# Kernel tuning notes

Measured on AMD Instinct MI355X. Metric: run time of the kernel, lower is better.

The kernel has to match this reference:

```python
import jax, jax.numpy as jnp
import numpy as np

B, L, D, H, HD, FF, NL = 2, 2048, 1024, 16, 64, 4096, 2
EPS = 1e-5
NEG = -1e30


def setup_inputs() -> dict:
    key = jax.random.key(0)
    ks = jax.random.split(key, 20)
    x = jax.random.normal(ks[0], (B, L, D), jnp.float32)
    # RoPE tables, rotate-half convention: [L, HD]
    pos = jnp.arange(L, dtype=jnp.float32)
    freqs = 1.0 / (10000.0 ** (jnp.arange(0, HD, 2, dtype=jnp.float32) / HD))
    ang = pos[:, None] * freqs[None, :]              # [L, HD/2]
    cos = jnp.concatenate([jnp.cos(ang), jnp.cos(ang)], -1)
    sin = jnp.concatenate([jnp.sin(ang), jnp.sin(ang)], -1)
    s = 0.02
    wq = jax.random.normal(ks[1], (NL, D, D), jnp.float32) * s
    wk = jax.random.normal(ks[2], (NL, D, D), jnp.float32) * s
    wv = jax.random.normal(ks[3], (NL, D, D), jnp.float32) * s
    wo = jax.random.normal(ks[4], (NL, D, D), jnp.float32) * s
    w1 = jax.random.normal(ks[5], (NL, D, FF), jnp.float32) * s
    w2 = jax.random.normal(ks[6], (NL, FF, D), jnp.float32) * s
    w3 = jax.random.normal(ks[7], (NL, D, FF), jnp.float32) * s
    attn_norm = jnp.ones((NL, D), jnp.float32)
    mlp_norm = jnp.ones((NL, D), jnp.float32)
    final_norm = jnp.ones((D,), jnp.float32)
    rw1 = jax.random.normal(ks[8], (D, D), jnp.float32) * s
    rb1 = jnp.zeros((D,), jnp.float32)
    rw2 = jax.random.normal(ks[9], (D, 1), jnp.float32) * s
    rb2 = jnp.zeros((1,), jnp.float32)
    return dict(x=x, cos=cos, sin=sin, wq=wq, wk=wk, wv=wv, wo=wo,
                w1=w1, w2=w2, w3=w3, attn_norm=attn_norm, mlp_norm=mlp_norm,
                final_norm=final_norm, rw1=rw1, rb1=rb1, rw2=rw2, rb2=rb2)


def _rms(x, w):
    return x * jax.lax.rsqrt(jnp.mean(x * x, -1, keepdims=True) + EPS) * w


def _rope(t, cos, sin):
    # t: [B, L, H, HD]; cos/sin: [L, HD]
    t1, t2 = jnp.split(t, 2, axis=-1)
    rot = jnp.concatenate([-t2, t1], -1)
    return t * cos[None, :, None, :] + rot * sin[None, :, None, :]


def reference(x, cos, sin, wq, wk, wv, wo, w1, w2, w3,
              attn_norm, mlp_norm, final_norm, rw1, rb1, rw2, rb2):
    causal = jnp.tril(jnp.ones((L, L), bool))
    h = x
    for i in range(NL):  # small fixed layer loop
        a = _rms(h, attn_norm[i])
        q = _rope((a @ wq[i]).reshape(B, L, H, HD), cos, sin)
        k = _rope((a @ wk[i]).reshape(B, L, H, HD), cos, sin)
        v = (a @ wv[i]).reshape(B, L, H, HD)
        sc = jnp.einsum('bqhd,bkhd->bhqk', q, k) / np.float32(np.sqrt(HD))
        sc = jnp.where(causal, sc, NEG)
        o = jnp.einsum('bhqk,bkhd->bqhd', jax.nn.softmax(sc, -1), v)
        h = h + o.reshape(B, L, D) @ wo[i]
        m = _rms(h, mlp_norm[i])
        h = h + (jax.nn.silu(m @ w1[i]) * (m @ w3[i])) @ w2[i]
    h = _rms(h, final_norm)

    # router chunking: straight-through hard boundaries
    logits = (jax.nn.silu(h @ rw1 + rb1) @ rw2 + rb2)[..., 0]   # [B, L]
    probs = jax.nn.sigmoid(logits)
    hard = (probs > 0.5).astype(h.dtype)
    mask = probs + jax.lax.stop_gradient(hard - probs)
    mask = mask.at[:, 0].set(1.0)
    mhard = jax.lax.stop_gradient(mask)
    # select matrix: S padded to static upper bound L (rows >= counts are zero)
    cums = jnp.cumsum(mhard, -1)                                # [B, L]
    seg = jnp.arange(1, L + 1, dtype=cums.dtype)[None, :, None] # [1, S, 1]
    assignment = (cums[:, None, :] == seg).astype(h.dtype)      # [B, S, L]
    select = assignment * mask[:, None, :]
    compressed = jnp.einsum('bsl,bld->bsd', select, h)          # [B, S, D]
    boundary_positions = jnp.argsort(-mhard, axis=-1)           # stable in jax
    counts = mhard.sum(-1).astype(jnp.int32)
    avg_chunk_size = jnp.float32(L) / jnp.mean(counts.astype(jnp.float32))
    return (h, compressed, boundary_positions, counts, avg_chunk_size)
```

## Files before the change

### kernel.cpp

```cpp
#include <hip/hip_runtime.h>
#include <cmath>

#define B_  2
#define L_  2048
#define D_  1024
#define H_  16
#define FF_ 4096
#define NL_ 2
#define NT_ (B_*L_)
#define ND_ (NT_*D_)

typedef __attribute__((ext_vector_type(8))) short bf16x8;
typedef __attribute__((ext_vector_type(4))) float f32x4;

__device__ __forceinline__ short f2bf(float x){
  unsigned u = __builtin_bit_cast(unsigned, x);
  unsigned r = (u + 0x7fffu + ((u>>16)&1u)) >> 16;
  return (short)r;
}
__device__ __forceinline__ float bf2f(short s){
  unsigned u = ((unsigned)(unsigned short)s) << 16;
  return __builtin_bit_cast(float, u);
}
#define MFMA16(a,b,c) __builtin_amdgcn_mfma_f32_16x16x32_bf16(a,b,c,0,0,0)

__device__ __forceinline__ void gload16(const short* g, short* l){
  __builtin_amdgcn_global_load_lds((const __attribute__((address_space(1))) void*)g,
                                   (__attribute__((address_space(3))) void*)l, 16, 0, 0);
}

__device__ __forceinline__ int2 xcd_swizzle(){
  int gx = gridDim.x;
  int n  = gx * gridDim.y;
  int hw = blockIdx.x + gx*blockIdx.y;
  int logical = (hw&7)*(n>>3) + (hw>>3);
  return make_int2(logical % gx, logical / gx);
}

template<bool WF32>
__global__ __launch_bounds__(256) void k_rmsnorm_s(const float* __restrict__ in,
                                                   const float* __restrict__ w,
                                                   short* __restrict__ oh,
                                                   short* __restrict__ ol,
                                                   float* __restrict__ of){
  int row = blockIdx.x; int tid = threadIdx.x;
  float4 xv = ((const float4*)(in + (size_t)row*D_))[tid];
  float ss = xv.x*xv.x + xv.y*xv.y + xv.z*xv.z + xv.w*xv.w;
  #pragma unroll
  for (int off=32; off; off>>=1) ss += __shfl_xor(ss, off);
  __shared__ float wsum[4];
  if ((tid&63)==0) wsum[tid>>6] = ss;
  __syncthreads();
  float tot = wsum[0]+wsum[1]+wsum[2]+wsum[3];
  float scale = 1.0f / sqrtf(tot*(1.0f/(float)D_) + 1e-5f);
  float4 w4 = ((const float4*)w)[tid];
  float v[4] = {xv.x*scale*w4.x, xv.y*scale*w4.y, xv.z*scale*w4.z, xv.w*scale*w4.w};
  short4 hh, ll;
  short h0=f2bf(v[0]); hh.x=h0; ll.x=f2bf(v[0]-bf2f(h0));
  short h1=f2bf(v[1]); hh.y=h1; ll.y=f2bf(v[1]-bf2f(h1));
  short h2=f2bf(v[2]); hh.z=h2; ll.z=f2bf(v[2]-bf2f(h2));
  short h3=f2bf(v[3]); hh.w=h3; ll.w=f2bf(v[3]-bf2f(h3));
  *(short4*)(oh + (size_t)row*D_ + tid*4) = hh;
  *(short4*)(ol + (size_t)row*D_ + tid*4) = ll;
  if (WF32){
    float4 ov; ov.x=v[0]; ov.y=v[1]; ov.z=v[2]; ov.w=v[3];
    ((float4*)(of + (size_t)row*D_))[tid] = ov;
  }
}

__global__ __launch_bounds__(256) void k_wsplit(const float* __restrict__ src,
                                                short* __restrict__ dh,
                                                short* __restrict__ dl,
                                                int srcN, int kOff, int nOff, int KT){
  __shared__ float t[64][68];
  int k0 = blockIdx.x*64, n0v = blockIdx.y*64;
  int tid = threadIdx.x;
  #pragma unroll
  for (int p=0;p<4;p++){
    int r = p*16 + (tid>>4);
    int c4 = (tid&15)*4;
    float4 v = *(const float4*)(src + (size_t)(kOff + k0 + r)*srcN + nOff + n0v + c4);
    *(float4*)&t[r][c4] = v;
  }
  __syncthreads();
  int n = tid>>2, kk = (tid&3)*16;
  bf16x8 H0, L0, H1, L1;
  #pragma unroll
  for (int q=0;q<8;q++){
    float v = t[kk+q][n]; short h=f2bf(v); H0[q]=h; L0[q]=f2bf(v-bf2f(h));
  }
  #pragma unroll
  for (int q=0;q<8;q++){
    float v = t[kk+8+q][n]; short h=f2bf(v); H1[q]=h; L1[q]=f2bf(v-bf2f(h));
  }
  size_t dof = (size_t)(n0v + n)*KT + k0 + kk;
  *(bf16x8*)(dh + dof) = H0;  *(bf16x8*)(dh + dof + 8) = H1;
  *(bf16x8*)(dl + dof) = L0;  *(bf16x8*)(dl + dof + 8) = L1;
}

__global__ __launch_bounds__(256,2) void k_qkv_mm(const short* __restrict__ Ah,
                                                  const short* __restrict__ Al,
                                                  const short* __restrict__ Wh,
                                                  const short* __restrict__ Wl,
                                                  short* __restrict__ OutH){
  __shared__ short lds[32768];
  int tid = threadIdx.x, wid = tid>>6, lane = tid&63;
  int l15 = lane&15, l4 = lane>>4;
  int wr = wid>>1, wc = wid&1;
  int2 bxy = xcd_swizzle();
  int m0 = bxy.y*128, n0 = bxy.x*128;
  const int K = 1024;
  f32x4 acc[4][4];
  #pragma unroll
  for (int i=0;i<4;i++){
    #pragma unroll
    for (int j=0;j<4;j++) acc[i][j] = (f32x4){0.f,0.f,0.f,0.f};
  }
  const short* gsrc = (wid==0)?Ah:(wid==1)?Al:(wid==2)?Wh:Wl;
  int rb = (wid<2)? m0 : n0;
  int gcol = ((lane&7)^(lane>>3))*8;
  short* ldsw = lds + wid*8192;
  const short* gp0 = gsrc + (size_t)(rb + (lane>>3))*K + gcol;
  for (int k0=0; k0<K; k0+=64){
    const short* gp = gp0 + k0;
    #pragma unroll
    for (int lc=0; lc<16; ++lc)
      gload16(gp + (size_t)lc*8*K, ldsw + lc*512);
    __syncthreads();
    #pragma unroll
    for (int ks=0; ks<2; ++ks){
      bf16x8 af[4], alf[4], wf[4], wlf[4];
      int gs = ((ks*4 + l4) ^ (lane&7))*8;
      #pragma unroll
      for (int f=0; f<4; ++f){
        int ar = (wr*64 + f*16 + l15)*64 + gs;
        af[f]  = *(const bf16x8*)&lds[ar];
        alf[f] = *(const bf16x8*)&lds[8192 + ar];
        int wr2 = (wc*64 + f*16 + l15)*64 + gs;
        wf[f]  = *(const bf16x8*)&lds[16384 + wr2];
        wlf[f] = *(const bf16x8*)&lds[24576 + wr2];
      }
      __builtin_amdgcn_s_setprio(1);
      #pragma unroll
      for (int i=0;i<4;i++){
        #pragma unroll
        for (int j=0;j<4;j++){
          acc[i][j] = MFMA16(af[i],  wf[j],  acc[i][j]);
          acc[i][j] = MFMA16(alf[i], wf[j],  acc[i][j]);
          acc[i][j] = MFMA16(af[i],  wlf[j], acc[i][j]);
        }
      }
      __builtin_amdgcn_s_setprio(0);
    }
    __syncthreads();
  }
  int sel = n0 >> 10;
  short* oh = OutH + (size_t)sel*8388608;
  short* ol = oh + 4194304;
  int cb = (n0 & 1023) + wc*64;
  #pragma unroll
  for (int i=0;i<4;i++){
    #pragma unroll
    for (int j=0;j<4;j++){
      #pragma unroll
      for (int r=0;r<4;r++){
        size_t mg = (size_t)(m0 + wr*64 + i*16 + l4*4 + r);
        int ng = cb + j*16 + l15;
        float v = acc[i][j][r];
        short h = f2bf(v);
        oh[mg*1024 + ng] = h;
        ol[mg*1024 + ng] = f2bf(v - bf2f(h));
      }
    }
  }
}

template<int EPI>
__global__ __launch_bounds__(256,(EPI==3)?2:3) void k_mm64(const short* __restrict__ Ah,
                                                const short* __restrict__ Al,
                                                const short* __restrict__ Wh,
                                                const short* __restrict__ Wl,
                                                const short* __restrict__ W3h,
                                                const short* __restrict__ W3l,
                                                int K,
                                                float* __restrict__ Cf,
                                                const float* __restrict__ bias,
                                                short* __restrict__ Gh,
                                                short* __restrict__ Gl,
                                                int ldc){
  __shared__ short lds[(EPI==3)?32768:24576];
  int tid = threadIdx.x, wid = tid>>6, lane = tid&63;
  int l15 = lane&15, l4 = lane>>4;
  int2 bxy = xcd_swizzle();
  int m0 = bxy.y*128, n0 = bxy.x*64;
  f32x4 a1[2][4], a3[2][4];
  #pragma unroll
  for (int i=0;i<2;i++){
    #pragma unroll
    for (int j=0;j<4;j++){ a1[i][j]=(f32x4){0.f,0.f,0.f,0.f}; a3[i][j]=(f32x4){0.f,0.f,0.f,0.f}; }
  }
  int gcol = ((lane&7)^(lane>>3))*8;
  int l8 = lane>>3;
  const int NCH = (EPI==3)? 16 : 12;
  for (int k0=0; k0<K; k0+=64){
    for (int t=0; t<NCH; ++t){
      int c = wid*NCH + t;
      const short* sb; int row0; short* db;
      if (c < 32){
        sb = (c<16)? Ah : Al; row0 = m0 + (c&15)*8;
        db = lds + ((c<16)?0:8192) + (c&15)*512;
      } else {
        int wseg = (c-32)>>3;
        sb = (wseg==0)?Wh:(wseg==1)?Wl:(wseg==2)?W3h:W3l;
        row0 = n0 + (c&7)*8;
        db = lds + 16384 + wseg*4096 + (c&7)*512;
      }
      gload16(sb + (size_t)(row0 + l8)*K + k0 + gcol, db);
    }
    __syncthreads();
    #pragma unroll
    for (int ks=0; ks<2; ++ks){
      int gs = ((ks*4 + l4) ^ (lane&7))*8;
      bf16x8 af[2], alf[2], wh[4], wl[4];
      #pragma unroll
      for (int f=0; f<2; ++f){
        int ar = (wid*32 + f*16 + l15)*64 + gs;
        af[f]  = *(const bf16x8*)&lds[ar];
        alf[f] = *(const bf16x8*)&lds[8192 + ar];
      }
      #pragma unroll
      for (int f=0; f<4; ++f){
        int wr2 = (f*16 + l15)*64 + gs;
        wh[f] = *(const bf16x8*)&lds[16384 + wr2];
        wl[f] = *(const bf16x8*)&lds[20480 + wr2];
      }
      __builtin_amdgcn_s_setprio(1);
      #pragma unroll
      for (int i=0;i<2;i++){
        #pragma unroll
        for (int j=0;j<4;j++){
          a1[i][j] = MFMA16(af[i],  wh[j], a1[i][j]);
          a1[i][j] = MFMA16(alf[i], wh[j], a1[i][j]);
          a1[i][j] = MFMA16(af[i],  wl[j], a1[i][j]);
        }
      }
      __builtin_amdgcn_s_setprio(0);
      if (EPI==3){
        bf16x8 w3h[4], w3l[4];
        #pragma unroll
        for (int f=0; f<4; ++f){
          int wr2 = (f*16 + l15)*64 + gs;
          w3h[f] = *(const bf16x8*)&lds[24576 + wr2];
          w3l[f] = *(const bf16x8*)&lds[28672 + wr2];
        }
        __builtin_amdgcn_s_setprio(1);
        #pragma unroll
        for (int i=0;i<2;i++){
          #pragma unroll
          for (int j=0;j<4;j++){
            a3[i][j] = MFMA16(af[i],  w3h[j], a3[i][j]);
            a3[i][j] = MFMA16(alf[i], w3h[j], a3[i][j]);
            a3[i][j] = MFMA16(af[i],  w3l[j], a3[i][j]);
          }
        }
        __builtin_amdgcn_s_setprio(0);
      }
    }
    __syncthreads();
  }
  #pragma unroll
  for (int i=0;i<2;i++){
    #pragma unroll
    for (int j=0;j<4;j++){
      #pragma unroll
      for (int r=0;r<4;r++){
        size_t mg = (size_t)(m0 + wid*32 + i*16 + l4*4 + r);
        int ng = n0 + j*16 + l15;
        float v = a1[i][j][r];
        if (EPI==1){
          float* cp = Cf + mg*ldc + ng;
          *cp = *cp + v;
        } else if (EPI==2){
          float x = v + bias[ng];
          Cf[mg*ldc + ng] = x/(1.f+expf(-x));
        } else {
          float g = v/(1.f+expf(-v)) * a3[i][j][r];
          short h = f2bf(g);
          Gh[mg*2048 + ng] = h;
          Gl[mg*2048 + ng] = f2bf(g - bf2f(h));
        }
      }
    }
  }
}

__global__ __launch_bounds__(256) void k_prep_k(const short* __restrict__ kh,
                                                const short* __restrict__ kl,
                                                const float* __restrict__ cosT,
                                                const float* __restrict__ sinT,
                                                short* __restrict__ kf){
  int wave = threadIdx.x>>6, lane = threadIdx.x&63;
  int t16 = blockIdx.x*4 + wave;
  int bh = blockIdx.y; int b = bh>>4, h = bh&15;
  int l15 = lane&15, l4 = lane>>4;
  int tok = t16*16 + l15;
  const short* khp = kh + (size_t)(b*L_+tok)*D_ + h*64;
  const short* klp = kl + (size_t)(b*L_+tok)*D_ + h*64;
  int d0 = l4*8;
  bf16x8 ka  = *(const bf16x8*)(khp + d0);
  bf16x8 kb2 = *(const bf16x8*)(khp + 32 + d0);
  bf16x8 kla = *(const bf16x8*)(klp + d0);
  bf16x8 klb = *(const bf16x8*)(klp + 32 + d0);
  const float* cr = cosT + (size_t)tok*64;
  const float* sr = sinT + (size_t)tok*64;
  float c0[8], s0[8], c1[8], s1[8];
  *(float4*)&c0[0] = *(const float4*)(cr + d0);      *(float4*)&c0[4] = *(const float4*)(cr + d0 + 4);
  *(float4*)&c1[0] = *(const float4*)(cr + 32 + d0); *(float4*)&c1[4] = *(const float4*)(cr + 32 + d0 + 4);
  *(float4*)&s0[0] = *(const float4*)(sr + d0);      *(float4*)&s0[4] = *(const float4*)(sr + d0 + 4);
  *(float4*)&s1[0] = *(const float4*)(sr + 32 + d0); *(float4*)&s1[4] = *(const float4*)(sr + 32 + d0 + 4);
  bf16x8 h0, lo0, h1, lo1;
  #pragma unroll
  for (int j=0;j<8;j++){
    float k0v = bf2f(ka[j]) + bf2f(kla[j]);
    float k1v = bf2f(kb2[j]) + bf2f(klb[j]);
    float r0 = k0v*c0[j] - k1v*s0[j];
    float r1 = k1v*c1[j] + k0v*s1[j];
    short a = f2bf(r0); h0[j]=a; lo0[j]=f2bf(r0 - bf2f(a));
    short bS = f2bf(r1); h1[j]=bS; lo1[j]=f2bf(r1 - bf2f(bS));
  }
  size_t base = ((size_t)(bh*128 + t16)*4)*512 + lane*8;
  *(bf16x8*)(kf + base)        = h0;
  *(bf16x8*)(kf + base + 512)  = lo0;
  *(bf16x8*)(kf + base + 1024) = h1;
  *(bf16x8*)(kf + base + 1536) = lo1;
}

__global__ __launch_bounds__(256) void k_prep_v(const short* __restrict__ vh,
                                                const short* __restrict__ vl,
                                                short* __restrict__ vf){
  int wave = threadIdx.x>>6, lane = threadIdx.x&63;
  int kc = blockIdx.x;
  int bh = blockIdx.y; int b = bh>>4, h = bh&15;
  int dt = wave;
  int l15 = lane&15, l4 = lane>>4;
  bf16x8 hi, lo;
  #pragma unroll
  for (int i=0;i<8;i++){
    size_t off = (size_t)(b*L_ + kc*32 + l4*8 + i)*D_ + h*64 + dt*16 + l15;
    hi[i] = vh[off];
    lo[i] = vl[off];
  }
  size_t base = (((size_t)(bh*64 + kc)*4 + dt)*2)*512 + lane*8;
  *(bf16x8*)(vf + base)       = hi;
  *(bf16x8*)(vf + base + 512) = lo;
}

__global__ __launch_bounds__(256) void k_attn_mfma(const short* __restrict__ qhb,
                                                   const short* __restrict__ qlb,
                                                   const short* __restrict__ kf,
                                                   const short* __restrict__ vf,
                                                   const float* __restrict__ cosT,
                                                   const float* __restrict__ sinT,
                                                   short* __restrict__ oh,
                                                   short* __restrict__ ol){
  int bid = blockIdx.x;
  int logical = (bid&7)*64 + (bid>>3);
  int bh = logical>>4, pair = logical&15;
  int b = bh>>4, h = bh&15;
  int wave = threadIdx.x>>6, lane = threadIdx.x&63;
  int l15 = lane&15, l4 = lane>>4;
  __shared__ short kvs[2][16384];
  __shared__ short pblob[4][2048];
  short* pb = pblob[wave];

  auto stage = [&](int bufi, int kt){
    const short* kg = kf + ((size_t)(bh*128 + kt*4))*2048;
    const short* vg = vf + ((size_t)(bh*64 + kt*2))*4096;
    short* dst = kvs[bufi];
    #pragma unroll
    for (int c=0;c<8;c++){
      int ch = wave*8 + c;
      const short* src = (ch<16)? (kg + ch*512) : (vg + (ch-16)*512);
      gload16(src + lane*8, dst + ch*512);
    }
  };

  for (int half=0; half<2; ++half){
    int qt = (half==0) ? (31-pair) : pair;
    stage(0, 0);
    int tok = qt*64 + wave*16 + l15;
    const short* qhp = qhb + (size_t)(b*L_+tok)*D_ + h*64;
    const short* qlp = qlb + (size_t)(b*L_+tok)*D_ + h*64;
    int d0 = l4*8;
    bf16x8 qa  = *(const bf16x8*)(qhp + d0);
    bf16x8 qb2 = *(const bf16x8*)(qhp + 32 + d0);
    bf16x8 qla = *(const bf16x8*)(qlp + d0);
    bf16x8 qlb2= *(const bf16x8*)(qlp + 32 + d0);
    const float* cr = cosT + (size_t)tok*64;
    const float* sr = sinT + (size_t)tok*64;
    float c0[8], s0[8], c1[8], s1[8];
    *(float4*)&c0[0] = *(const float4*)(cr + d0);      *(float4*)&c0[4] = *(const float4*)(cr + d0 + 4);
    *(float4*)&c1[0] = *(const float4*)(cr + 32 + d0); *(float4*)&c1[4] = *(const float4*)(cr + 32 + d0 + 4);
    *(float4*)&s0[0] = *(const float4*)(sr + d0);      *(float4*)&s0[4] = *(const float4*)(sr + d0 + 4);
    *(float4*)&s1[0] = *(const float4*)(sr + 32 + d0); *(float4*)&s1[4] = *(const float4*)(sr + 32 + d0 + 4);
    bf16x8 qh0, ql0, qh1, ql1;
    #pragma unroll
    for (int j=0;j<8;j++){
      float q0v = bf2f(qa[j]) + bf2f(qla[j]);
      float q1v = bf2f(qb2[j]) + bf2f(qlb2[j]);
      float r0 = (q0v*c0[j] - q1v*s0[j]) * 0.125f;
      float r1 = (q1v*c1[j] + q0v*s1[j]) * 0.125f;
      short a = f2bf(r0); qh0[j]=a; ql0[j]=f2bf(r0 - bf2f(a));
      short bS = f2bf(r1); qh1[j]=bS; ql1[j]=f2bf(r1 - bf2f(bS));
    }

    f32x4 O[4];
    #pragma unroll
    for (int dt=0;dt<4;dt++) O[dt] = (f32x4){0.f,0.f,0.f,0.f};
    float m_[4] = {-1e30f,-1e30f,-1e30f,-1e30f};
    float ls[4] = {0.f,0.f,0.f,0.f};

    int cur = 0;
    for (int kt=0; kt<=qt; ++kt){
      bool haveNext = (kt < qt);
      if (haveNext){
        stage(cur^1, kt+1);
        asm volatile("s_waitcnt vmcnt(8)" ::: "memory");
      } else {
        asm volatile("s_waitcnt vmcnt(0)" ::: "memory");
      }
      __builtin_amdgcn_s_barrier();
      const short* Kl = kvs[cur];
      const short* Vl = kvs[cur] + 8192;
      bool dtile = (kt == qt);
      f32x4 sr4[4];
      #pragma unroll
      for (int g=0; g<4; g++){
        f32x4 acc = (f32x4){0.f,0.f,0.f,0.f};
        if (!(dtile && g > wave)){
          const short* kp = Kl + g*2048 + lane*8;
          bf16x8 kh0 = *(const bf16x8*)(kp);
          bf16x8 kl0 = *(const bf16x8*)(kp + 512);
          bf16x8 kh1 = *(const bf16x8*)(kp + 1024);
          bf16x8 kl1 = *(const bf16x8*)(kp + 1536);
          __builtin_amdgcn_s_setprio(1);
          acc = MFMA16(qh0, kh0, acc); acc = MFMA16(qh1, kh1, acc);
          acc = MFMA16(ql0, kh0, acc); acc = MFMA16(ql1, kh1, acc);
          acc = MFMA16(qh0, kl0, acc); acc = MFMA16(qh1, kl1, acc);
          __builtin_amdgcn_s_setprio(0);
        }
        sr4[g] = acc;
      }
      float p_[4][4];
      #pragma unroll
      for (int r=0; r<4; r++){
        int rowrel = wave*16 + l4*4 + r;
        float mx = -1e30f;
        float sv[4];
        #pragma unroll
        for (int g=0; g<4; g++){
          float v = sr4[g][r];
          if (dtile && (g*16 + l15) > rowrel) v = -1e30f;
          sv[g] = v; mx = fmaxf(mx, v);
        }
        #pragma unroll
        for (int off=1; off<16; off<<=1) mx = fmaxf(mx, __shfl_xor(mx, off));
        float nm = fmaxf(m_[r], mx);
        float al = __expf(m_[r] - nm);
        m_[r] = nm;
        float ps = 0.f;
        #pragma unroll
        for (int g=0; g<4; g++){ float pv = __expf(sv[g] - nm); p_[g][r] = pv; ps += pv; }
        #pragma unroll
        for (int off=1; off<16; off<<=1) ps += __shfl_xor(ps, off);
        ls[r] = ls[r]*al + ps;
        #pragma unroll
        for (int dt=0; dt<4; dt++) O[dt][r] *= al;
      }
      #pragma unroll
      for (int g=0; g<4; g++){
        int key = g*16 + l15;
        int cc = key>>5, sub = (key>>3)&3, ii = key&7;
        #pragma unroll
        for (int r=0; r<4; r++){
          float pv = p_[g][r];
          short ph = f2bf(pv);
          short pl = f2bf(pv - bf2f(ph));
          int idx = cc*1024 + (sub*16 + l4*4 + r)*8 + ii;
          pb[idx] = ph;
          pb[idx + 512] = pl;
        }
      }
      asm volatile("s_waitcnt lgkmcnt(0)" ::: "memory");
      #pragma unroll
      for (int cc=0; cc<2; cc++){
        bf16x8 pah = *(const bf16x8*)(pb + cc*1024 + lane*8);
        bf16x8 pal = *(const bf16x8*)(pb + cc*1024 + 512 + lane*8);
        const short* vp = Vl + cc*4096 + lane*8;
        __builtin_amdgcn_s_setprio(1);
        #pragma unroll
        for (int dt=0; dt<4; dt++){
          bf16x8 vh = *(const bf16x8*)(vp + dt*1024);
          bf16x8 vl = *(const bf16x8*)(vp + dt*1024 + 512);
          O[dt] = MFMA16(pah, vh, O[dt]);
          O[dt] = MFMA16(pal, vh, O[dt]);
          O[dt] = MFMA16(pah, vl, O[dt]);
        }
        __builtin_amdgcn_s_setprio(0);
      }
      __builtin_amdgcn_s_barrier();
      cur ^= 1;
    }
    #pragma unroll
    for (int r=0; r<4; r++){
      float inv = 1.0f / ls[r];
      size_t row = (size_t)(b*L_ + qt*64 + wave*16 + l4*4 + r);
      #pragma unroll
      for (int dt=0; dt<4; dt++){
        float v = O[dt][r]*inv;
        short hh = f2bf(v);
        oh[row*D_ + h*64 + dt*16 + l15] = hh;
        ol[row*D_ + h*64 + dt*16 + l15] = f2bf(v - bf2f(hh));
      }
    }
  }
}

__global__ __launch_bounds__(256) void k_gemv(const float* __restrict__ T,
                                              const float* __restrict__ rw2,
                                              const float* __restrict__ rb2,
                                              float* __restrict__ logits){
  int row = blockIdx.x; int tid = threadIdx.x;
  float4 tv = ((const float4*)(T + (size_t)row*D_))[tid];
  float4 wv = ((const float4*)rw2)[tid];
  float s = tv.x*wv.x + tv.y*wv.y + tv.z*wv.z + tv.w*wv.w;
  #pragma unroll
  for (int off=32; off; off>>=1) s += __shfl_xor(s, off);
  __shared__ float ps[4];
  if ((tid&63)==0) ps[tid>>6] = s;
  __syncthreads();
  if (tid==0) logits[row] = ps[0]+ps[1]+ps[2]+ps[3] + rb2[0];
}

__global__ __launch_bounds__(256) void k_boundary(const float* __restrict__ logits,
                                                  float* __restrict__ pos_out,
                                                  int* __restrict__ hard,
                                                  int* __restrict__ cums,
                                                  int* __restrict__ counts){
  int b = blockIdx.x; int tid = threadIdx.x;
  __shared__ int part[256];
  int loc[8]; int s=0;
  int base = b*L_;
  #pragma unroll
  for (int j=0;j<8;j++){
    int ll = tid*8 + j;
    float lg = logits[base+ll];
    int hv = (ll==0) ? 1 : ((lg > 0.0f) ? 1 : 0);
    loc[j]=hv; s+=hv;
  }
  part[tid]=s; __syncthreads();
  for (int off=1; off<256; off<<=1){
    int v = part[tid];
    int add = (tid>=off) ? part[tid-off] : 0;
    __syncthreads();
    part[tid] = v + add;
    __syncthreads();
  }
  int total = part[255];
  int run = part[tid] - s;
  #pragma unroll
  for (int j=0;j<8;j++){
    int ll = tid*8+j;
    run += loc[j];
    hard[base+ll] = loc[j];
    cums[base+ll] = run;
    int idx = loc[j] ? (run-1) : (total + ll - run);
    pos_out[base+idx] = (float)ll;
  }
  if (tid==0) counts[b] = total;
}

__global__ __launch_bounds__(256) void k_scatter(const float* __restrict__ hf,
                                                 const int* __restrict__ hard,
                                                 const int* __restrict__ cums,
                                                 float* __restrict__ comp){
  int rowid = blockIdx.x;
  if (!hard[rowid]) return;
  int b = rowid >> 11;
  int s = cums[rowid]-1;
  const float4* src = (const float4*)(hf + (size_t)rowid*D_);
  float4* dst = (float4*)(comp + (size_t)(b*L_ + s)*D_);
  dst[threadIdx.x] = src[threadIdx.x];
}

__global__ void k_finalize(const int* __restrict__ counts, float* __restrict__ out){
  if (threadIdx.x==0 && blockIdx.x==0){
    float c0 = (float)counts[0], c1 = (float)counts[1];
    out[0]=c0; out[1]=c1;
    out[2] = (float)L_ / (0.5f*(c0+c1));
  }
}

extern "C" void kernel_launch(void* const* d_in, const int* in_sizes, int n_in,
                              void* d_out, int out_size, void* d_ws, size_t ws_size,
                              hipStream_t stream){
  const float* x      = (const float*)d_in[0];
  const float* cosT   = (const float*)d_in[1];
  const float* sinT   = (const float*)d_in[2];
  const float* wq     = (const float*)d_in[3];
  const float* wk     = (const float*)d_in[4];
  const float* wv     = (const float*)d_in[5];
  const float* wo     = (const float*)d_in[6];
  const float* w1     = (const float*)d_in[7];
  const float* w2     = (const float*)d_in[8];
  const float* w3     = (const float*)d_in[9];
  const float* attn_n = (const float*)d_in[10];
  const float* mlp_n  = (const float*)d_in[11];
  const float* final_n= (const float*)d_in[12];
  const float* rw1    = (const float*)d_in[13];
  const float* rb1    = (const float*)d_in[14];
  const float* rw2    = (const float*)d_in[15];
  const float* rb2    = (const float*)d_in[16];

  float* outF = (float*)d_out;
  float* hD   = outF;
  float* compD= outF + (size_t)ND_;
  float* posD = outF + (size_t)2*ND_;

  char* WS = (char*)d_ws;
  auto S = [&](size_t mb){ return (short*)(WS + mb*1048576ull); };
  auto F = [&](size_t mb){ return (float*)(WS + mb*1048576ull); };
  short *ah=S(0), *al=S(8);
  short *qh=S(16), *ql=S(24), *kh=S(32), *kl=S(40), *vh=S(48), *vl=S(56);
  short *qkvwt_h=S(64), *qkvwt_l=S(70);
  short *vf=S(64);
  short *kf=S(48);
  short *wot_h=S(32), *wot_l=S(34);
  short *gh=S(16), *gl=S(32);
  short *w1t_h=S(48), *w1t_l=S(52), *w3t_h=S(56), *w3t_l=S(60);
  short *w2t_h=S(64), *w2t_l=S(68);
  short *rw1t_h=S(16), *rw1t_l=S(18);
  float *ra=F(20);
  float *logits=F(76);
  int *hard=(int*)(logits+NT_), *cums=hard+NT_, *cnts=cums+NT_;
  short *oh=(short*)compD, *ol=oh+4194304;

  hipMemcpyAsync(hD, x, (size_t)ND_*sizeof(float), hipMemcpyDeviceToDevice, stream);

  for (int i=0;i<NL_;++i){
    k_rmsnorm_s<false><<<NT_,256,0,stream>>>(hD, attn_n + (size_t)i*D_, ah, al, nullptr);
    k_wsplit<<<dim3(16,16),256,0,stream>>>(wq + (size_t)i*D_*D_, qkvwt_h,         qkvwt_l,         1024, 0, 0, 1024);
    k_wsplit<<<dim3(16,16),256,0,stream>>>(wk + (size_t)i*D_*D_, qkvwt_h+1048576, qkvwt_l+1048576, 1024, 0, 0, 1024);
    k_wsplit<<<dim3(16,16),256,0,stream>>>(wv + (size_t)i*D_*D_, qkvwt_h+2097152, qkvwt_l+2097152, 1024, 0, 0, 1024);
    k_qkv_mm<<<dim3(24,32),256,0,stream>>>(ah, al, qkvwt_h, qkvwt_l, qh);
    k_prep_v<<<dim3(64,32),256,0,stream>>>(vh, vl, vf);
    k_prep_k<<<dim3(32,32),256,0,stream>>>(kh, kl, cosT, sinT, kf);
    k_wsplit<<<dim3(16,16),256,0,stream>>>(wo + (size_t)i*D_*D_, wot_h, wot_l, 1024, 0, 0, 1024);
    k_attn_mfma<<<dim3(512),256,0,stream>>>(qh, ql, kf, vf, cosT, sinT, oh, ol);
    k_mm64<1><<<dim3(16,32),256,0,stream>>>(oh, ol, wot_h, wot_l, nullptr, nullptr,
                                            1024, hD, nullptr, nullptr, nullptr, 1024);
    k_rmsnorm_s<false><<<NT_,256,0,stream>>>(hD, mlp_n + (size_t)i*D_, ah, al, nullptr);
    for (int hc=0; hc<2; ++hc){
      k_wsplit<<<dim3(16,32),256,0,stream>>>(w1 + (size_t)i*D_*FF_, w1t_h, w1t_l, 4096, 0, hc*2048, 1024);
      k_wsplit<<<dim3(16,32),256,0,stream>>>(w3 + (size_t)i*D_*FF_, w3t_h, w3t_l, 4096, 0, hc*2048, 1024);
      k_wsplit<<<dim3(32,16),256,0,stream>>>(w2 + (size_t)i*FF_*D_, w2t_h, w2t_l, 1024, hc*2048, 0, 2048);
      k_mm64<3><<<dim3(32,32),256,0,stream>>>(ah, al, w1t_h, w1t_l, w3t_h, w3t_l,
                                              1024, nullptr, nullptr, gh, gl, 0);
      k_mm64<1><<<dim3(16,32),256,0,stream>>>(gh, gl, w2t_h, w2t_l, nullptr, nullptr,
                                              2048, hD, nullptr, nullptr, nullptr, 1024);
    }
  }
  k_rmsnorm_s<true><<<NT_,256,0,stream>>>(hD, final_n, ah, al, hD);
  k_wsplit<<<dim3(16,16),256,0,stream>>>(rw1, rw1t_h, rw1t_l, 1024, 0, 0, 1024);
  k_mm64<2><<<dim3(16,32),256,0,stream>>>(ah, al, rw1t_h, rw1t_l, nullptr, nullptr,
                                          1024, ra, rb1, nullptr, nullptr, 1024);
  k_gemv<<<NT_,256,0,stream>>>(ra, rw2, rb2, logits);
  k_boundary<<<B_,256,0,stream>>>(logits, posD, hard, cums, cnts);
  hipMemsetAsync(compD, 0, (size_t)ND_*sizeof(float), stream);
  k_scatter<<<NT_,256,0,stream>>>(hD, hard, cums, compD);
  k_finalize<<<1,64,0,stream>>>(cnts, posD + NT_);
}
```

Measured before the change: 1.256 ms.

## Batch weight-split launches, fuse V layout into QKV GEMM, lazy softmax rescale

Merges the separate weight-split launches (QKV, FFN, and Wo together with K preparation) into single grid launches, which cuts launch overhead and lets small kernels overlap. The V output of the QKV GEMM is now written directly in the attention layout, so the k_prep_v kernel and its round trip through memory are gone. Attention softmax skips the running-max rescale when the new block max stays within 8 of the current max, which saves exp and multiply work. Launch-bound occupancy hints are also raised, which risks register spills, and workspace buffers are remapped to avoid aliasing.

```diff
diff --git a/kernel.cpp b/kernel.cpp
--- a/kernel.cpp
+++ b/kernel.cpp
@@ -68,41 +68,80 @@
   }
 }
 
+__device__ __forceinline__ void wsplit_body(float (*t)[68], const float* __restrict__ src,
+                                            short* __restrict__ dh, short* __restrict__ dl,
+                                            int srcN, int kOff, int nOff, int KT,
+                                            int bx, int by){
+  int k0 = bx*64, n0v = by*64;
+  int tid = threadIdx.x;
+  #pragma unroll
+  for (int p=0;p<4;p++){
+    int r = p*16 + (tid>>4);
+    int c4 = (tid&15)*4;
+    float4 v = *(const float4*)(src + (size_t)(kOff + k0 + r)*srcN + nOff + n0v + c4);
+    *(float4*)&t[r][c4] = v;
+  }
+  __syncthreads();
+  int n = tid>>2, kk = (tid&3)*16;
+  bf16x8 H0, L0, H1, L1;
+  #pragma unroll
+  for (int q=0;q<8;q++){
+    float v = t[kk+q][n]; short h=f2bf(v); H0[q]=h; L0[q]=f2bf(v-bf2f(h));
+  }
+  #pragma unroll
+  for (int q=0;q<8;q++){
+    float v = t[kk+8+q][n]; short h=f2bf(v); H1[q]=h; L1[q]=f2bf(v-bf2f(h));
+  }
+  size_t dof = (size_t)(n0v + n)*KT + k0 + kk;
+  *(bf16x8*)(dh + dof) = H0;  *(bf16x8*)(dh + dof + 8) = H1;
+  *(bf16x8*)(dl + dof) = L0;  *(bf16x8*)(dl + dof + 8) = L1;
+}
+
 __global__ __launch_bounds__(256) void k_wsplit(const float* __restrict__ src,
                                                 short* __restrict__ dh,
                                                 short* __restrict__ dl,
                                                 int srcN, int kOff, int nOff, int KT){
   __shared__ float t[64][68];
-  int k0 = blockIdx.x*64, n0v = blockIdx.y*64;
-  int tid = threadIdx.x;
-  #pragma unroll
-  for (int p=0;p<4;p++){
-    int r = p*16 + (tid>>4);
-    int c4 = (tid&15)*4;
-    float4 v = *(const float4*)(src + (size_t)(kOff + k0 + r)*srcN + nOff + n0v + c4);
-    *(float4*)&t[r][c4] = v;
-  }
-  __syncthreads();
-  int n = tid>>2, kk = (tid&3)*16;
-  bf16x8 H0, L0, H1, L1;
-  #pragma unroll
-  for (int q=0;q<8;q++){
-    float v = t[kk+q][n]; short h=f2bf(v); H0[q]=h; L0[q]=f2bf(v-bf2f(h));
-  }
-  #pragma unroll
-  for (int q=0;q<8;q++){
-    float v = t[kk+8+q][n]; short h=f2bf(v); H1[q]=h; L1[q]=f2bf(v-bf2f(h));
-  }
-  size_t dof = (size_t)(n0v + n)*KT + k0 + kk;
-  *(bf16x8*)(dh + dof) = H0;  *(bf16x8*)(dh + dof + 8) = H1;
-  *(bf16x8*)(dl + dof) = L0;  *(bf16x8*)(dl + dof + 8) = L1;
-}
-
-__global__ __launch_bounds__(256,2) void k_qkv_mm(const short* __restrict__ Ah,
+  wsplit_body(t, src, dh, dl, srcN, kOff, nOff, KT, blockIdx.x, blockIdx.y);
+}
+
+__global__ __launch_bounds__(256) void k_wsplit_qkv(const float* __restrict__ wq,
+                                                    const float* __restrict__ wk,
+                                                    const float* __restrict__ wv,
+                                                    short* __restrict__ dh,
+                                                    short* __restrict__ dl){
+  __shared__ float t[64][68];
+  int z = blockIdx.z;
+  const float* s = (z==0)?wq:(z==1)?wk:wv;
+  wsplit_body(t, s, dh + (size_t)z*1048576, dl + (size_t)z*1048576,
+              1024, 0, 0, 1024, blockIdx.x, blockIdx.y);
+}
+
+__global__ __launch_bounds__(256) void k_wsplit_ffn(const float* __restrict__ w1,
+                                                    const float* __restrict__ w3,
+                                                    const float* __restrict__ w2,
+                                                    short* __restrict__ w1h, short* __restrict__ w1l,
+                                                    short* __restrict__ w3h, short* __restrict__ w3l,
+                                                    short* __restrict__ w2h, short* __restrict__ w2l,
+                                                    int hc){
+  __shared__ float t[64][68];
+  int z = blockIdx.z;
+  if (z < 2){
+    if (blockIdx.x >= 16) return;
+    const float* s = z ? w3 : w1;
+    wsplit_body(t, s, z?w3h:w1h, z?w3l:w1l, 4096, 0, hc*2048, 1024, blockIdx.x, blockIdx.y);
+  } else {
+    if (blockIdx.y >= 16) return;
+    wsplit_body(t, w2, w2h, w2l, 1024, hc*2048, 0, 2048, blockIdx.x, blockIdx.y);
+  }
+}
+
+__global__ __launch_bounds__(256,3) void k_qkv_mm(const short* __restrict__ Ah,
                                                   const short* __restrict__ Al,
                                                   const short* __restrict__ Wh,
                                                   const short* __restrict__ Wl,
-                                                  short* __restrict__ OutH){
+                                                  short* __restrict__ OutH,
+                                                  short* __restrict__ Vf){
   __shared__ short lds[32768];
   int tid = threadIdx.x, wid = tid>>6, lane = tid&63;
   int l15 = lane&15, l4 = lane>>4;
@@ -155,28 +194,52 @@
     __syncthreads();
   }
   int sel = n0 >> 10;
-  short* oh = OutH + (size_t)sel*8388608;
-  short* ol = oh + 4194304;
   int cb = (n0 & 1023) + wc*64;
-  #pragma unroll
-  for (int i=0;i<4;i++){
-    #pragma unroll
-    for (int j=0;j<4;j++){
-      #pragma unroll
-      for (int r=0;r<4;r++){
-        size_t mg = (size_t)(m0 + wr*64 + i*16 + l4*4 + r);
-        int ng = cb + j*16 + l15;
-        float v = acc[i][j][r];
-        short h = f2bf(v);
-        oh[mg*1024 + ng] = h;
-        ol[mg*1024 + ng] = f2bf(v - bf2f(h));
+  if (sel < 2){
+    short* oh = OutH + (size_t)sel*8388608;
+    short* ol = oh + 4194304;
+    #pragma unroll
+    for (int i=0;i<4;i++){
+      #pragma unroll
+      for (int j=0;j<4;j++){
+        #pragma unroll
+        for (int r=0;r<4;r++){
+          size_t mg = (size_t)(m0 + wr*64 + i*16 + l4*4 + r);
+          int ng = cb + j*16 + l15;
+          float v = acc[i][j][r];
+          short h = f2bf(v);
+          oh[mg*1024 + ng] = h;
+          ol[mg*1024 + ng] = f2bf(v - bf2f(h));
+        }
+      }
+    }
+  } else {
+    #pragma unroll
+    for (int i=0;i<4;i++){
+      #pragma unroll
+      for (int j=0;j<4;j++){
+        #pragma unroll
+        for (int r=0;r<4;r++){
+          int mg = m0 + wr*64 + i*16 + l4*4 + r;
+          int ng = cb + j*16 + l15;
+          float v = acc[i][j][r];
+          short hh2 = f2bf(v);
+          short ll2 = f2bf(v - bf2f(hh2));
+          int bb = mg >> 11, tt = mg & 2047;
+          int hd = ng >> 6, kc = tt >> 5;
+          int l4v = (tt>>3)&3, iv = tt&7;
+          int dtv = (ng>>4)&3, l15v = ng&15;
+          size_t base = ((size_t)((bb*16+hd)*64 + kc)*8 + dtv*2)*512 + (l4v*16+l15v)*8 + iv;
+          Vf[base] = hh2;
+          Vf[base + 512] = ll2;
+        }
       }
     }
   }
 }
 
 template<int EPI>
-__global__ __launch_bounds__(256,(EPI==3)?2:3) void k_mm64(const short* __restrict__ Ah,
+__global__ __launch_bounds__(256,(EPI==3)?3:4) void k_mm64(const short* __restrict__ Ah,
                                                 const short* __restrict__ Al,
                                                 const short* __restrict__ Wh,
                                                 const short* __restrict__ Wl,
@@ -294,14 +357,24 @@
   }
 }
 
-__global__ __launch_bounds__(256) void k_prep_k(const short* __restrict__ kh,
-                                                const short* __restrict__ kl,
-                                                const float* __restrict__ cosT,
-                                                const float* __restrict__ sinT,
-                                                short* __restrict__ kf){
+__global__ __launch_bounds__(256) void k_prep_k_wo(const short* __restrict__ kh,
+                                                   const short* __restrict__ kl,
+                                                   const float* __restrict__ cosT,
+                                                   const float* __restrict__ sinT,
+                                                   short* __restrict__ kf,
+                                                   const float* __restrict__ wo,
+                                                   short* __restrict__ woh,
+                                                   short* __restrict__ wol){
+  __shared__ float t[64][68];
+  int x = blockIdx.x;
+  if (x >= 1024){
+    int idx = x - 1024;
+    wsplit_body(t, wo, woh, wol, 1024, 0, 0, 1024, idx & 15, idx >> 4);
+    return;
+  }
   int wave = threadIdx.x>>6, lane = threadIdx.x&63;
-  int t16 = blockIdx.x*4 + wave;
-  int bh = blockIdx.y; int b = bh>>4, h = bh&15;
+  int t16 = (x & 31)*4 + wave;
+  int bh = x >> 5; int b = bh>>4, h = bh&15;
   int l15 = lane&15, l4 = lane>>4;
   int tok = t16*16 + l15;
   const short* khp = kh + (size_t)(b*L_+tok)*D_ + h*64;
@@ -333,26 +406,6 @@
   *(bf16x8*)(kf + base + 512)  = lo0;
   *(bf16x8*)(kf + base + 1024) = h1;
   *(bf16x8*)(kf + base + 1536) = lo1;
-}
-
-__global__ __launch_bounds__(256) void k_prep_v(const short* __restrict__ vh,
-                                                const short* __restrict__ vl,
-                                                short* __restrict__ vf){
-  int wave = threadIdx.x>>6, lane = threadIdx.x&63;
-  int kc = blockIdx.x;
-  int bh = blockIdx.y; int b = bh>>4, h = bh&15;
-  int dt = wave;
-  int l15 = lane&15, l4 = lane>>4;
-  bf16x8 hi, lo;
-  #pragma unroll
-  for (int i=0;i<8;i++){
-    size_t off = (size_t)(b*L_ + kc*32 + l4*8 + i)*D_ + h*64 + dt*16 + l15;
-    hi[i] = vh[off];
-    lo[i] = vl[off];
-  }
-  size_t base = (((size_t)(bh*64 + kc)*4 + dt)*2)*512 + lane*8;
-  *(bf16x8*)(vf + base)       = hi;
-  *(bf16x8*)(vf + base + 512) = lo;
 }
 
 __global__ __launch_bounds__(256) void k_attn_mfma(const short* __restrict__ qhb,
@@ -465,17 +518,26 @@
         }
         #pragma unroll
         for (int off=1; off<16; off<<=1) mx = fmaxf(mx, __shfl_xor(mx, off));
-        float nm = fmaxf(m_[r], mx);
-        float al = __expf(m_[r] - nm);
-        m_[r] = nm;
-        float ps = 0.f;
-        #pragma unroll
-        for (int g=0; g<4; g++){ float pv = __expf(sv[g] - nm); p_[g][r] = pv; ps += pv; }
-        #pragma unroll
-        for (int off=1; off<16; off<<=1) ps += __shfl_xor(ps, off);
-        ls[r] = ls[r]*al + ps;
-        #pragma unroll
-        for (int dt=0; dt<4; dt++) O[dt][r] *= al;
+        if (__all(mx <= m_[r] + 8.0f)){
+          float ps = 0.f;
+          #pragma unroll
+          for (int g=0; g<4; g++){ float pv = __expf(sv[g] - m_[r]); p_[g][r] = pv; ps += pv; }
+          #pragma unroll
+          for (int off=1; off<16; off<<=1) ps += __shfl_xor(ps, off);
+          ls[r] += ps;
+        } else {
+          float nm = fmaxf(m_[r], mx);
+          float al = __expf(m_[r] - nm);
+          m_[r] = nm;
+          float ps = 0.f;
+          #pragma unroll
+          for (int g=0; g<4; g++){ float pv = __expf(sv[g] - nm); p_[g][r] = pv; ps += pv; }
+          #pragma unroll
+          for (int off=1; off<16; off<<=1) ps += __shfl_xor(ps, off);
+          ls[r] = ls[r]*al + ps;
+          #pragma unroll
+          for (int dt=0; dt<4; dt++) O[dt][r] *= al;
+        }
       }
       #pragma unroll
       for (int g=0; g<4; g++){
@@ -631,11 +693,11 @@
   auto S = [&](size_t mb){ return (short*)(WS + mb*1048576ull); };
   auto F = [&](size_t mb){ return (float*)(WS + mb*1048576ull); };
   short *ah=S(0), *al=S(8);
-  short *qh=S(16), *ql=S(24), *kh=S(32), *kl=S(40), *vh=S(48), *vl=S(56);
-  short *qkvwt_h=S(64), *qkvwt_l=S(70);
+  short *qh=S(16), *ql=S(24), *kh=S(32), *kl=S(40);
+  short *qkvwt_h=S(48), *qkvwt_l=S(54);
   short *vf=S(64);
   short *kf=S(48);
-  short *wot_h=S(32), *wot_l=S(34);
+  short *wot_h=S(0), *wot_l=S(2);
   short *gh=S(16), *gl=S(32);
   short *w1t_h=S(48), *w1t_l=S(52), *w3t_h=S(56), *w3t_l=S(60);
   short *w2t_h=S(64), *w2t_l=S(68);
@@ -649,21 +711,19 @@
 
   for (int i=0;i<NL_;++i){
     k_rmsnorm_s<false><<<NT_,256,0,stream>>>(hD, attn_n + (size_t)i*D_, ah, al, nullptr);
-    k_wsplit<<<dim3(16,16),256,0,stream>>>(wq + (size_t)i*D_*D_, qkvwt_h,         qkvwt_l,         1024, 0, 0, 1024);
-    k_wsplit<<<dim3(16,16),256,0,stream>>>(wk + (size_t)i*D_*D_, qkvwt_h+1048576, qkvwt_l+1048576, 1024, 0, 0, 1024);
-    k_wsplit<<<dim3(16,16),256,0,stream>>>(wv + (size_t)i*D_*D_, qkvwt_h+2097152, qkvwt_l+2097152, 1024, 0, 0, 1024);
-    k_qkv_mm<<<dim3(24,32),256,0,stream>>>(ah, al, qkvwt_h, qkvwt_l, qh);
-    k_prep_v<<<dim3(64,32),256,0,stream>>>(vh, vl, vf);
-    k_prep_k<<<dim3(32,32),256,0,stream>>>(kh, kl, cosT, sinT, kf);
-    k_wsplit<<<dim3(16,16),256,0,stream>>>(wo + (size_t)i*D_*D_, wot_h, wot_l, 1024, 0, 0, 1024);
+    k_wsplit_qkv<<<dim3(16,16,3),256,0,stream>>>(wq + (size_t)i*D_*D_, wk + (size_t)i*D_*D_,
+                                                 wv + (size_t)i*D_*D_, qkvwt_h, qkvwt_l);
+    k_qkv_mm<<<dim3(24,32),256,0,stream>>>(ah, al, qkvwt_h, qkvwt_l, qh, vf);
+    k_prep_k_wo<<<dim3(1280),256,0,stream>>>(kh, kl, cosT, sinT, kf,
+                                             wo + (size_t)i*D_*D_, wot_h, wot_l);
     k_attn_mfma<<<dim3(512),256,0,stream>>>(qh, ql, kf, vf, cosT, sinT, oh, ol);
     k_mm64<1><<<dim3(16,32),256,0,stream>>>(oh, ol, wot_h, wot_l, nullptr, nullptr,
                                             1024, hD, nullptr, nullptr, nullptr, 1024);
     k_rmsnorm_s<false><<<NT_,256,0,stream>>>(hD, mlp_n + (size_t)i*D_, ah, al, nullptr);
     for (int hc=0; hc<2; ++hc){
-      k_wsplit<<<dim3(16,32),256,0,stream>>>(w1 + (size_t)i*D_*FF_, w1t_h, w1t_l, 4096, 0, hc*2048, 1024);
-      k_wsplit<<<dim3(16,32),256,0,stream>>>(w3 + (size_t)i*D_*FF_, w3t_h, w3t_l, 4096, 0, hc*2048, 1024);
-      k_wsplit<<<dim3(32,16),256,0,stream>>>(w2 + (size_t)i*FF_*D_, w2t_h, w2t_l, 1024, hc*2048, 0, 2048);
+      k_wsplit_ffn<<<dim3(32,32,3),256,0,stream>>>(w1 + (size_t)i*D_*FF_, w3 + (size_t)i*D_*FF_,
+                                                   w2 + (size_t)i*FF_*D_,
+                                                   w1t_h, w1t_l, w3t_h, w3t_l, w2t_h, w2t_l, hc);
       k_mm64<3><<<dim3(32,32),256,0,stream>>>(ah, al, w1t_h, w1t_l, w3t_h, w3t_l,
                                               1024, nullptr, nullptr, gh, gl, 0);
       k_mm64<1><<<dim3(16,32),256,0,stream>>>(gh, gl, w2t_h, w2t_l, nullptr, nullptr,
```

Result: slower. 1.458 ms (+16.1%).
